# Kernel tuning notes

Measured on AMD Instinct MI355X. Metric: run time of the kernel, lower is better.

The kernel has to match this reference:

```python
import jax, jax.numpy as jnp
import numpy as np

N_NODES = 50000
N_EDGES = 800000
IN_CH = 128
OUT_CH = 64
HEADS = 4
NEG_SLOPE = 0.2


def setup_inputs() -> dict:
    key = jax.random.key(0)
    k1, k2, k3, k4, k5 = jax.random.split(key, 5)
    x = jax.random.normal(k1, (N_NODES, IN_CH), dtype=jnp.float32)
    edge_index = jax.random.randint(k2, (2, N_EDGES), 0, N_NODES, dtype=jnp.int64)
    # Glorot-ish scaled params
    W = jax.random.normal(k3, (IN_CH, HEADS * OUT_CH), dtype=jnp.float32) * (1.0 / np.sqrt(IN_CH))
    att_src = jax.random.normal(k4, (HEADS, OUT_CH), dtype=jnp.float32) * (1.0 / np.sqrt(OUT_CH))
    att_dst = jax.random.normal(k5, (HEADS, OUT_CH), dtype=jnp.float32) * (1.0 / np.sqrt(OUT_CH))
    bias = jnp.zeros((HEADS * OUT_CH,), dtype=jnp.float32)
    return {"x": x, "edge_index": edge_index, "W": W, "att_src": att_src, "att_dst": att_dst, "bias": bias}


def reference(x, edge_index, W, att_src, att_dst, bias):
    N = x.shape[0]
    H, C = att_src.shape
    # PyG GATConv default add_self_loops=True
    loops = jnp.arange(N, dtype=edge_index.dtype)
    src = jnp.concatenate([edge_index[0], loops])  # message source j
    dst = jnp.concatenate([edge_index[1], loops])  # message target i
    # Linear transform per head: [N, H, C]
    h = (x @ W).reshape(N, H, C)
    # Per-node attention logits: [N, H]
    a_src = jnp.sum(h * att_src[None], axis=-1)
    a_dst = jnp.sum(h * att_dst[None], axis=-1)
    # Per-edge raw score (alpha_src from source node, alpha_dst from target node)
    e = jax.nn.leaky_relu(a_src[src] + a_dst[dst], NEG_SLOPE)  # [E, H]
    # Segment-softmax over incoming edges of each target node
    m = jax.ops.segment_max(e, dst, num_segments=N)  # [N, H]
    m = jnp.where(jnp.isfinite(m), m, 0.0)  # nodes with no edges -> 0
    ex = jnp.exp(e - m[dst])
    denom = jax.ops.segment_sum(ex, dst, num_segments=N)  # [N, H]
    alpha = ex / (denom[dst] + 1e-16)  # [E, H]
    # Weighted aggregate of source features: [N, H, C]
    msg = h[src] * alpha[:, :, None]
    out = jax.ops.segment_sum(msg, dst, num_segments=N)
    # concat=True: flatten heads, add bias
    return out.reshape(N, H * C) + bias
```

## Files before the change

### kernel.cpp

```cpp
#include <hip/hip_runtime.h>

#define N_NODES 50000
#define N_EDGES 800000
#define IN_CH 128
#define OUT_CH 64
#define HEADS 4
#define HC 256
#define NEG_SLOPE 0.2f
#define GEMM_BLOCKS 782
#define COUNT_BLOCKS 782
#define SCAN_BLOCKS 49

#define HB_OFF       0UL
#define WSW_OFF      25600000UL
#define ASRC_OFF     25665536UL
#define ADST_OFF     26465536UL
#define COUNTS_OFF   27265536UL
#define OFFSETS_OFF  27465536UL
#define CURSOR_OFF   27665536UL
#define BSUMS_OFF    27865536UL
#define SIDX_OFF     27866560UL
#define EXV_OFF      31066560UL

typedef __attribute__((ext_vector_type(8))) short short8;
typedef __attribute__((ext_vector_type(4))) float f32x4;
typedef __attribute__((ext_vector_type(2))) __fp16 fp16x2;

__device__ __forceinline__ unsigned short f2bf(float f) {
  unsigned int u = __float_as_uint(f);
  unsigned int r = (u + 0x7fffu + ((u >> 16) & 1u)) >> 16;
  return (unsigned short)r;
}
__device__ __forceinline__ unsigned f2h2(float a, float b) {
  fp16x2 h = __builtin_amdgcn_cvt_pkrtz(a, b);
  return __builtin_bit_cast(unsigned, h);
}
__device__ __forceinline__ void fma2(float& a0, float& a1, unsigned u, float e) {
  fp16x2 h = __builtin_bit_cast(fp16x2, u);
  a0 = fmaf((float)h.x, e, a0);
  a1 = fmaf((float)h.y, e, a1);
}
__device__ __forceinline__ float lrelu(float e) {
  return e > 0.f ? e : NEG_SLOPE * e;
}

__global__ __launch_bounds__(256) void init_k(const float* __restrict__ W,
                                              unsigned short* __restrict__ Wsw,
                                              int* __restrict__ counts) {
  if (blockIdx.x < 16) {
    int idx = blockIdx.x * 256 + threadIdx.x;
    int l = idx & 63;
    int kc = (idx >> 6) & 3;
    int t = idx >> 8;
    int kbase = kc * 32 + (l >> 4) * 8;
    int col = t * 16 + (l & 15);
    unsigned int p[4];
#pragma unroll
    for (int j = 0; j < 4; ++j) {
      unsigned int lo = f2bf(W[(size_t)(kbase + 2 * j) * HC + col]);
      unsigned int hi = f2bf(W[(size_t)(kbase + 2 * j + 1) * HC + col]);
      p[j] = lo | (hi << 16);
    }
    *(uint4*)(Wsw + (size_t)idx * 8) = make_uint4(p[0], p[1], p[2], p[3]);
  } else {
    int i = (blockIdx.x - 16) * 256 + threadIdx.x;
    if (i < N_NODES) counts[i] = 0;
  }
}

__global__ __launch_bounds__(256) void gemm_count(const float* __restrict__ x,
                                                  const unsigned short* __restrict__ Wsw,
                                                  const float* __restrict__ att_s,
                                                  const float* __restrict__ att_d,
                                                  const int* __restrict__ dstv,
                                                  unsigned short* __restrict__ hb,
                                                  float* __restrict__ a_src,
                                                  float* __restrict__ a_dst,
                                                  int* __restrict__ counts) {
  __shared__ float Cs[4][16][256];

  if (blockIdx.x >= GEMM_BLOCKS) {
    int base = (blockIdx.x - GEMM_BLOCKS) * 1024 + threadIdx.x;
#pragma unroll
    for (int k = 0; k < 4; ++k) {
      int e = base + k * 256;
      if (e < N_EDGES) atomicAdd(&counts[dstv[e]], 1);
    }
    return;
  }

  const int wave = threadIdx.x >> 6;
  const int l = threadIdx.x & 63;
  const int q = l >> 4;
  const int m = l & 15;
  const int mrow = blockIdx.x * 64 + wave * 16 + m;
  const bool mvalid = mrow < N_NODES;
  const int rc = mvalid ? mrow : (N_NODES - 1);

  short8 a[4];
  const float* xr = x + (size_t)rc * IN_CH + q * 8;
#pragma unroll
  for (int kc = 0; kc < 4; ++kc) {
    float4 u = *(const float4*)(xr + kc * 32);
    float4 v = *(const float4*)(xr + kc * 32 + 4);
    short8 t;
    t[0] = (short)f2bf(u.x); t[1] = (short)f2bf(u.y);
    t[2] = (short)f2bf(u.z); t[3] = (short)f2bf(u.w);
    t[4] = (short)f2bf(v.x); t[5] = (short)f2bf(v.y);
    t[6] = (short)f2bf(v.z); t[7] = (short)f2bf(v.w);
    a[kc] = t;
  }

#pragma unroll
  for (int t = 0; t < 16; ++t) {
    f32x4 acc = {0.f, 0.f, 0.f, 0.f};
#pragma unroll
    for (int kc = 0; kc < 4; ++kc) {
      short8 b = *(const short8*)(Wsw + ((size_t)(t * 4 + kc) * 64 + l) * 8);
      acc = __builtin_amdgcn_mfma_f32_16x16x32_bf16(a[kc], b, acc, 0, 0, 0);
    }
#pragma unroll
    for (int r = 0; r < 4; ++r) {
      int row = q * 4 + r;
      Cs[wave][row][(t * 16 + m) ^ (row << 2)] = acc[r];
    }
  }
  __syncthreads();

  float as = 0.f, ad = 0.f;
  unsigned short* hrow = hb + (size_t)mrow * HC + q * 64;
  const int sw = m << 2;
#pragma unroll
  for (int i = 0; i < 8; ++i) {
    int col0 = q * 64 + i * 8;
    float4 c1 = *(const float4*)&Cs[wave][m][(col0) ^ sw];
    float4 c2 = *(const float4*)&Cs[wave][m][(col0 + 4) ^ sw];
    float4 s1 = *(const float4*)(att_s + col0);
    float4 s2 = *(const float4*)(att_s + col0 + 4);
    float4 d1 = *(const float4*)(att_d + col0);
    float4 d2 = *(const float4*)(att_d + col0 + 4);
    as += c1.x * s1.x + c1.y * s1.y + c1.z * s1.z + c1.w * s1.w;
    as += c2.x * s2.x + c2.y * s2.y + c2.z * s2.z + c2.w * s2.w;
    ad += c1.x * d1.x + c1.y * d1.y + c1.z * d1.z + c1.w * d1.w;
    ad += c2.x * d2.x + c2.y * d2.y + c2.z * d2.z + c2.w * d2.w;
    if (mvalid) {
      uint4 p;
      p.x = f2h2(c1.x, c1.y);
      p.y = f2h2(c1.z, c1.w);
      p.z = f2h2(c2.x, c2.y);
      p.w = f2h2(c2.z, c2.w);
      *(uint4*)(hrow + i * 8) = p;
    }
  }
  if (mvalid) {
    a_src[mrow * HEADS + q] = as;
    a_dst[mrow * HEADS + q] = ad;
  }
}

__global__ __launch_bounds__(256) void scan1(const int* __restrict__ counts,
                                             int* __restrict__ offsets,
                                             int* __restrict__ bsums) {
  __shared__ int sd[256];
  const int base = blockIdx.x * 1024;
  const int t = threadIdx.x;
  int v[4];
  int tsum = 0;
#pragma unroll
  for (int k = 0; k < 4; ++k) {
    int i = base + t * 4 + k;
    v[k] = (i < N_NODES) ? counts[i] : 0;
    tsum += v[k];
  }
  sd[t] = tsum;
  __syncthreads();
  for (int off = 1; off < 256; off <<= 1) {
    int xval = (t >= off) ? sd[t - off] : 0;
    __syncthreads();
    sd[t] += xval;
    __syncthreads();
  }
  int excl = sd[t] - tsum;
  int run = excl;
#pragma unroll
  for (int k = 0; k < 4; ++k) {
    int i = base + t * 4 + k;
    if (i < N_NODES) offsets[i] = run;
    run += v[k];
  }
  if (t == 255) bsums[blockIdx.x] = sd[255];
}

__global__ __launch_bounds__(256) void scan23(int* __restrict__ offsets,
                                              const int* __restrict__ bsums,
                                              int* __restrict__ cursor) {
  __shared__ int s_add;
  if (threadIdx.x < 64) {
    int lane = threadIdx.x;
    int v = (lane < SCAN_BLOCKS) ? bsums[lane] : 0;
#pragma unroll
    for (int o = 1; o < 64; o <<= 1) {
      int t = __shfl_up(v, o);
      if (lane >= o) v += t;
    }
    int b = blockIdx.x;
    int pre = (b == 0) ? 0 : __shfl(v, b - 1);
    if (lane == 0) s_add = pre;
  }
  __syncthreads();
  const int add = s_add;
  const int base = blockIdx.x * 1024;
  const int t = threadIdx.x;
#pragma unroll
  for (int k = 0; k < 4; ++k) {
    int i = base + t * 4 + k;
    if (i < N_NODES) {
      int o = offsets[i] + add;
      offsets[i] = o;
      cursor[i] = o;
    }
  }
}

__global__ __launch_bounds__(256) void scatter_k(const int* __restrict__ src,
                                                 const int* __restrict__ dst,
                                                 const float* __restrict__ a_src,
                                                 const float* __restrict__ a_dst,
                                                 int* __restrict__ cursor,
                                                 int* __restrict__ sidx,
                                                 float* __restrict__ exv) {
  int e = blockIdx.x * 256 + threadIdx.x;
  if (e < N_EDGES) {
    int s = src[e];
    int d = dst[e];
    float4 as = *(const float4*)(a_src + s * 4);
    float4 ad = *(const float4*)(a_dst + d * 4);
    float4 ex;
    ex.x = __expf(lrelu(as.x + ad.x));
    ex.y = __expf(lrelu(as.y + ad.y));
    ex.z = __expf(lrelu(as.z + ad.z));
    ex.w = __expf(lrelu(as.w + ad.w));
    int pos = atomicAdd(&cursor[d], 1);
    sidx[pos] = s;
    *(float4*)(exv + (size_t)pos * 4) = ex;
  }
}

__global__ __launch_bounds__(256) void aggregate(const unsigned short* __restrict__ hb,
                                                 const float* __restrict__ a_src,
                                                 const float* __restrict__ a_dst,
                                                 const int* __restrict__ counts,
                                                 const int* __restrict__ offsets,
                                                 const int* __restrict__ sidx,
                                                 const float* __restrict__ exv,
                                                 const float* __restrict__ bias,
                                                 float* __restrict__ out) {
  const int node = blockIdx.x * 4 + (threadIdx.x >> 6);
  const int l = threadIdx.x & 63;
  const int g = l >> 4;
  const int q = l & 15;
  const int hd = q >> 2;
  const int cb = q * 32;
  const int deg = counts[node];
  const int start = offsets[node];
  const char* hbase = (const char*)hb;

  float denom = 0.f;
  float acc[16];
#pragma unroll
  for (int k = 0; k < 16; ++k) acc[k] = 0.f;

  for (int j = 0; j + g < deg; j += 8) {
    int i0 = start + j + g;
    bool v1 = (j + g + 4) < deg;
    int i1 = v1 ? (i0 + 4) : i0;
    int s0 = sidx[i0];
    int s1 = sidx[i1];
    float ex0 = exv[(size_t)i0 * 4 + hd];
    float ex1 = v1 ? exv[(size_t)i1 * 4 + hd] : 0.f;
    const char* hp0 = hbase + (size_t)s0 * 512 + cb;
    const char* hp1 = hbase + (size_t)s1 * 512 + cb;
    uint4 A0 = *(const uint4*)hp0;
    uint4 A1 = *(const uint4*)(hp0 + 16);
    uint4 B0 = *(const uint4*)hp1;
    uint4 B1 = *(const uint4*)(hp1 + 16);
    denom += ex0 + ex1;
    fma2(acc[0],  acc[1],  A0.x, ex0);  fma2(acc[2],  acc[3],  A0.y, ex0);
    fma2(acc[4],  acc[5],  A0.z, ex0);  fma2(acc[6],  acc[7],  A0.w, ex0);
    fma2(acc[8],  acc[9],  A1.x, ex0);  fma2(acc[10], acc[11], A1.y, ex0);
    fma2(acc[12], acc[13], A1.z, ex0);  fma2(acc[14], acc[15], A1.w, ex0);
    fma2(acc[0],  acc[1],  B0.x, ex1);  fma2(acc[2],  acc[3],  B0.y, ex1);
    fma2(acc[4],  acc[5],  B0.z, ex1);  fma2(acc[6],  acc[7],  B0.w, ex1);
    fma2(acc[8],  acc[9],  B1.x, ex1);  fma2(acc[10], acc[11], B1.y, ex1);
    fma2(acc[12], acc[13], B1.z, ex1);  fma2(acc[14], acc[15], B1.w, ex1);
  }

  denom += __shfl_xor(denom, 16);
  denom += __shfl_xor(denom, 32);
#pragma unroll
  for (int k = 0; k < 16; ++k) {
    acc[k] += __shfl_xor(acc[k], 16);
    acc[k] += __shfl_xor(acc[k], 32);
  }

  float es = a_src[node * HEADS + hd] + a_dst[node * HEADS + hd];
  float exs = __expf(lrelu(es));
  denom += exs;
  const char* hp = hbase + (size_t)node * 512 + cb;
  uint4 h0 = *(const uint4*)hp;
  uint4 h1 = *(const uint4*)(hp + 16);
  fma2(acc[0],  acc[1],  h0.x, exs);  fma2(acc[2],  acc[3],  h0.y, exs);
  fma2(acc[4],  acc[5],  h0.z, exs);  fma2(acc[6],  acc[7],  h0.w, exs);
  fma2(acc[8],  acc[9],  h1.x, exs);  fma2(acc[10], acc[11], h1.y, exs);
  fma2(acc[12], acc[13], h1.z, exs);  fma2(acc[14], acc[15], h1.w, exs);

  float inv = 1.f / (denom + 1e-16f);
  int c = q * 16 + g * 4;
  float4 bv = *(const float4*)(bias + c);
  float4 o = make_float4(acc[g * 4 + 0] * inv + bv.x, acc[g * 4 + 1] * inv + bv.y,
                         acc[g * 4 + 2] * inv + bv.z, acc[g * 4 + 3] * inv + bv.w);
  *(float4*)(out + (size_t)node * HC + c) = o;
}

extern "C" void kernel_launch(void* const* d_in, const int* in_sizes, int n_in,
                              void* d_out, int out_size, void* d_ws, size_t ws_size,
                              hipStream_t stream) {
  const float* x     = (const float*)d_in[0];
  const int*   ei    = (const int*)d_in[1];
  const float* W     = (const float*)d_in[2];
  const float* att_s = (const float*)d_in[3];
  const float* att_d = (const float*)d_in[4];
  const float* bias  = (const float*)d_in[5];
  float* out = (float*)d_out;

  char* ws = (char*)d_ws;
  unsigned short* hb  = (unsigned short*)(ws + HB_OFF);
  unsigned short* Wsw = (unsigned short*)(ws + WSW_OFF);
  float* a_src  = (float*)(ws + ASRC_OFF);
  float* a_dst  = (float*)(ws + ADST_OFF);
  int* counts   = (int*)(ws + COUNTS_OFF);
  int* offsets  = (int*)(ws + OFFSETS_OFF);
  int* cursor   = (int*)(ws + CURSOR_OFF);
  int* bsums    = (int*)(ws + BSUMS_OFF);
  int* sidx     = (int*)(ws + SIDX_OFF);
  float* exv    = (float*)(ws + EXV_OFF);

  const int* src = ei;
  const int* dst = ei + N_EDGES;

  init_k<<<16 + 196, 256, 0, stream>>>(W, Wsw, counts);
  gemm_count<<<GEMM_BLOCKS + COUNT_BLOCKS, 256, 0, stream>>>(
      x, Wsw, att_s, att_d, dst, hb, a_src, a_dst, counts);
  scan1<<<SCAN_BLOCKS, 256, 0, stream>>>(counts, offsets, bsums);
  scan23<<<SCAN_BLOCKS, 256, 0, stream>>>(offsets, bsums, cursor);
  scatter_k<<<3125, 256, 0, stream>>>(src, dst, a_src, a_dst, cursor, sidx, exv);
  aggregate<<<12500, 256, 0, stream>>>(hb, a_src, a_dst, counts, offsets, sidx, exv, bias, out);
}
```

Before: 246.9 us.

## Record edge rank during counting to drop scatter atomics; switch GEMM to fp16

The counting pass now stores the return value of each atomic increment as a per-edge rank. The scatter pass then computes each edge's CSR position as offsets[dst] + rank with no second round of atomics, and the cursor array goes away. Separately, the GEMM converts x and W to fp16 with packed conversion and uses the f16 MFMA instead of bf16 with manual rounding, which cuts conversion ALU work. The cost is an extra 3.2MB rank array written and read back, plus a narrower exponent range for fp16, which could overflow on unusual inputs.

```diff
diff --git a/kernel.cpp b/kernel.cpp
--- a/kernel.cpp
+++ b/kernel.cpp
@@ -17,20 +17,17 @@
 #define ADST_OFF     26465536UL
 #define COUNTS_OFF   27265536UL
 #define OFFSETS_OFF  27465536UL
-#define CURSOR_OFF   27665536UL
-#define BSUMS_OFF    27865536UL
-#define SIDX_OFF     27866560UL
-#define EXV_OFF      31066560UL
+#define BSUMS_OFF    27665536UL
+#define RANK_OFF     27666560UL
+#define SIDX_OFF     30866560UL
+#define EXV_OFF      34066560UL
 
 typedef __attribute__((ext_vector_type(8))) short short8;
+typedef __attribute__((ext_vector_type(8))) __fp16 f16x8;
+typedef __attribute__((ext_vector_type(4))) unsigned uint32x4;
 typedef __attribute__((ext_vector_type(4))) float f32x4;
 typedef __attribute__((ext_vector_type(2))) __fp16 fp16x2;
 
-__device__ __forceinline__ unsigned short f2bf(float f) {
-  unsigned int u = __float_as_uint(f);
-  unsigned int r = (u + 0x7fffu + ((u >> 16) & 1u)) >> 16;
-  return (unsigned short)r;
-}
 __device__ __forceinline__ unsigned f2h2(float a, float b) {
   fp16x2 h = __builtin_amdgcn_cvt_pkrtz(a, b);
   return __builtin_bit_cast(unsigned, h);
@@ -57,9 +54,8 @@
     unsigned int p[4];
 #pragma unroll
     for (int j = 0; j < 4; ++j) {
-      unsigned int lo = f2bf(W[(size_t)(kbase + 2 * j) * HC + col]);
-      unsigned int hi = f2bf(W[(size_t)(kbase + 2 * j + 1) * HC + col]);
-      p[j] = lo | (hi << 16);
+      p[j] = f2h2(W[(size_t)(kbase + 2 * j) * HC + col],
+                  W[(size_t)(kbase + 2 * j + 1) * HC + col]);
     }
     *(uint4*)(Wsw + (size_t)idx * 8) = make_uint4(p[0], p[1], p[2], p[3]);
   } else {
@@ -76,7 +72,8 @@
                                                   unsigned short* __restrict__ hb,
                                                   float* __restrict__ a_src,
                                                   float* __restrict__ a_dst,
-                                                  int* __restrict__ counts) {
+                                                  int* __restrict__ counts,
+                                                  int* __restrict__ rank) {
   __shared__ float Cs[4][16][256];
 
   if (blockIdx.x >= GEMM_BLOCKS) {
@@ -84,7 +81,7 @@
 #pragma unroll
     for (int k = 0; k < 4; ++k) {
       int e = base + k * 256;
-      if (e < N_EDGES) atomicAdd(&counts[dstv[e]], 1);
+      if (e < N_EDGES) rank[e] = atomicAdd(&counts[dstv[e]], 1);
     }
     return;
   }
@@ -97,18 +94,18 @@
   const bool mvalid = mrow < N_NODES;
   const int rc = mvalid ? mrow : (N_NODES - 1);
 
-  short8 a[4];
+  f16x8 a[4];
   const float* xr = x + (size_t)rc * IN_CH + q * 8;
 #pragma unroll
   for (int kc = 0; kc < 4; ++kc) {
     float4 u = *(const float4*)(xr + kc * 32);
     float4 v = *(const float4*)(xr + kc * 32 + 4);
-    short8 t;
-    t[0] = (short)f2bf(u.x); t[1] = (short)f2bf(u.y);
-    t[2] = (short)f2bf(u.z); t[3] = (short)f2bf(u.w);
-    t[4] = (short)f2bf(v.x); t[5] = (short)f2bf(v.y);
-    t[6] = (short)f2bf(v.z); t[7] = (short)f2bf(v.w);
-    a[kc] = t;
+    uint32x4 t;
+    t[0] = f2h2(u.x, u.y);
+    t[1] = f2h2(u.z, u.w);
+    t[2] = f2h2(v.x, v.y);
+    t[3] = f2h2(v.z, v.w);
+    a[kc] = __builtin_bit_cast(f16x8, t);
   }
 
 #pragma unroll
@@ -116,8 +113,8 @@
     f32x4 acc = {0.f, 0.f, 0.f, 0.f};
 #pragma unroll
     for (int kc = 0; kc < 4; ++kc) {
-      short8 b = *(const short8*)(Wsw + ((size_t)(t * 4 + kc) * 64 + l) * 8);
-      acc = __builtin_amdgcn_mfma_f32_16x16x32_bf16(a[kc], b, acc, 0, 0, 0);
+      f16x8 b = *(const f16x8*)(Wsw + ((size_t)(t * 4 + kc) * 64 + l) * 8);
+      acc = __builtin_amdgcn_mfma_f32_16x16x32_f16(a[kc], b, acc, 0, 0, 0);
     }
 #pragma unroll
     for (int r = 0; r < 4; ++r) {
@@ -192,8 +189,7 @@
 }
 
 __global__ __launch_bounds__(256) void scan23(int* __restrict__ offsets,
-                                              const int* __restrict__ bsums,
-                                              int* __restrict__ cursor) {
+                                              const int* __restrict__ bsums) {
   __shared__ int s_add;
   if (threadIdx.x < 64) {
     int lane = threadIdx.x;
@@ -214,19 +210,16 @@
 #pragma unroll
   for (int k = 0; k < 4; ++k) {
     int i = base + t * 4 + k;
-    if (i < N_NODES) {
-      int o = offsets[i] + add;
-      offsets[i] = o;
-      cursor[i] = o;
-    }
+    if (i < N_NODES) offsets[i] += add;
   }
 }
 
 __global__ __launch_bounds__(256) void scatter_k(const int* __restrict__ src,
                                                  const int* __restrict__ dst,
+                                                 const int* __restrict__ rank,
+                                                 const int* __restrict__ offsets,
                                                  const float* __restrict__ a_src,
                                                  const float* __restrict__ a_dst,
-                                                 int* __restrict__ cursor,
                                                  int* __restrict__ sidx,
                                                  float* __restrict__ exv) {
   int e = blockIdx.x * 256 + threadIdx.x;
@@ -240,7 +233,7 @@
     ex.y = __expf(lrelu(as.y + ad.y));
     ex.z = __expf(lrelu(as.z + ad.z));
     ex.w = __expf(lrelu(as.w + ad.w));
-    int pos = atomicAdd(&cursor[d], 1);
+    int pos = offsets[d] + rank[e];
     sidx[pos] = s;
     *(float4*)(exv + (size_t)pos * 4) = ex;
   }
@@ -340,8 +333,8 @@
   float* a_dst  = (float*)(ws + ADST_OFF);
   int* counts   = (int*)(ws + COUNTS_OFF);
   int* offsets  = (int*)(ws + OFFSETS_OFF);
-  int* cursor   = (int*)(ws + CURSOR_OFF);
   int* bsums    = (int*)(ws + BSUMS_OFF);
+  int* rank     = (int*)(ws + RANK_OFF);
   int* sidx     = (int*)(ws + SIDX_OFF);
   float* exv    = (float*)(ws + EXV_OFF);
 
@@ -350,9 +343,9 @@
 
   init_k<<<16 + 196, 256, 0, stream>>>(W, Wsw, counts);
   gemm_count<<<GEMM_BLOCKS + COUNT_BLOCKS, 256, 0, stream>>>(
-      x, Wsw, att_s, att_d, dst, hb, a_src, a_dst, counts);
+      x, Wsw, att_s, att_d, dst, hb, a_src, a_dst, counts, rank);
   scan1<<<SCAN_BLOCKS, 256, 0, stream>>>(counts, offsets, bsums);
-  scan23<<<SCAN_BLOCKS, 256, 0, stream>>>(offsets, bsums, cursor);
-  scatter_k<<<3125, 256, 0, stream>>>(src, dst, a_src, a_dst, cursor, sidx, exv);
+  scan23<<<SCAN_BLOCKS, 256, 0, stream>>>(offsets, bsums);
+  scatter_k<<<3125, 256, 0, stream>>>(src, dst, rank, offsets, a_src, a_dst, sidx, exv);
   aggregate<<<12500, 256, 0, stream>>>(hb, a_src, a_dst, counts, offsets, sidx, exv, bias, out);
 }
```

Measured after the change: 233.5 us. 1.06x faster.
